# Performance work log

Measured on AMD Instinct MI355X. Metric: run time of the kernel, lower is better.

Reference implementation:

```python
import jax, jax.numpy as jnp
import numpy as np

S, D, A, H, C = 2048, 256, 64, 8, 64  # seq_len, node_dim, num_aux, num_heads, num_channels
QUAT = 4
N_TYPES = 3  # nodes, aux, rot


def _linear_params(key, out_dim, in_dim, use_bias=True):
    kw, kb = jax.random.split(key)
    lim = 1.0 / np.sqrt(in_dim)
    W = jax.random.uniform(kw, (out_dim, in_dim), minval=-lim, maxval=lim, dtype=jnp.float32)
    if not use_bias:
        return W, None
    b = jax.random.uniform(kb, (out_dim,), minval=-lim, maxval=lim, dtype=jnp.float32)
    return W, b


def setup_inputs() -> dict:
    key = jax.random.key(0)
    ks = jax.random.split(key, 8)
    nodes = jax.random.normal(ks[0], (S, D), dtype=jnp.float32)
    aux = jax.random.normal(ks[1], (S, A), dtype=jnp.float32)
    rot = jax.random.normal(ks[2], (S, QUAT), dtype=jnp.float32)
    W_nodes, b_nodes = _linear_params(ks[3], H * C * 2, D)
    W_aux, b_aux = _linear_params(ks[4], H * C * 2, A)
    W_rot, _ = _linear_params(ks[5], H * C * 2, QUAT, use_bias=False)
    W_val, b_val = _linear_params(ks[6], D * H * N_TYPES, D)
    return {
        "nodes": nodes, "aux": aux, "rot": rot,
        "W_nodes": W_nodes, "b_nodes": b_nodes,
        "W_aux": W_aux, "b_aux": b_aux,
        "W_rot": W_rot,
        "W_val": W_val, "b_val": b_val,
    }


def reference(nodes, aux, rot, W_nodes, b_nodes, W_aux, b_aux, W_rot, W_val, b_val):
    seq_len = nodes.shape[0]
    # values: (S, 3H, D)
    val = (nodes @ W_val.T + b_val).reshape(seq_len, N_TYPES * H, -1)
    # per-source k/q: each (S, H, C)
    nodes_k, nodes_q = jnp.split((nodes @ W_nodes.T + b_nodes).reshape(seq_len, H, -1), 2, -1)
    aux_k, aux_q = jnp.split((aux @ W_aux.T + b_aux).reshape(seq_len, H, -1), 2, -1)
    rot_k, rot_q = jnp.split((rot @ W_rot.T).reshape(seq_len, H, -1), 2, -1)
    # concat along head axis -> (S, 3H, C)
    k = jnp.concatenate([nodes_k, aux_k, rot_k], axis=-2)
    q = jnp.concatenate([nodes_q, aux_q, rot_q], axis=-2)
    # (S, S, 3H) score tensor, scaled by 1/sqrt(num_heads) as in the original
    logits = jnp.einsum('ihc,jhc->ijh', k, q) / jnp.sqrt(jnp.asarray(H, nodes.dtype))
    att = jax.nn.softmax(logits, axis=-2)  # softmax over the j (key) axis
    out = jnp.einsum('ijh,jhd->id', att, val)  # (S, D)
    return out
```

## Files before the change

### kernel.cpp

```cpp
#include <hip/hip_runtime.h>

#define S_LEN 2048
#define NHEAD 24
#define CDIM 64
#define DDIM 256

typedef _Float16 f16x8 __attribute__((ext_vector_type(8)));
typedef float f32x4 __attribute__((ext_vector_type(4)));

__device__ __forceinline__ ushort f2h(float f) {
    _Float16 h = (_Float16)f;
    return __builtin_bit_cast(ushort, h);
}
__device__ __forceinline__ uint pkh(float a, float b) {
    auto v = __builtin_amdgcn_cvt_pkrtz(a, b);
    return __builtin_bit_cast(uint, v);
}
__device__ __forceinline__ uint pk2(float a, float b) {
    return (uint)f2h(a) | ((uint)f2h(b) << 16);
}

__device__ __forceinline__ int4 cvt8(const float* __restrict__ p) {
    float4 a = *(const float4*)p;
    float4 b = *(const float4*)(p + 4);
    f16x8 h;
    h[0] = (_Float16)a.x; h[1] = (_Float16)a.y;
    h[2] = (_Float16)a.z; h[3] = (_Float16)a.w;
    h[4] = (_Float16)b.x; h[5] = (_Float16)b.y;
    h[6] = (_Float16)b.z; h[7] = (_Float16)b.w;
    return __builtin_bit_cast(int4, h);
}

__global__ __launch_bounds__(256) void prep_kernel(
    const float* __restrict__ nodes, const float* __restrict__ W_val,
    float* __restrict__ out, ushort* __restrict__ nodes16, ushort* __restrict__ Wval16)
{
    int idx = blockIdx.x * 256 + threadIdx.x;
    if (idx < 131072) {
        ((float4*)out)[idx] = float4{0.f, 0.f, 0.f, 0.f};
    } else if (idx < 196608) {
        int i = idx - 131072;
        *(int4*)&nodes16[i * 8] = cvt8(&nodes[i * 8]);
    } else {
        int i = idx - 196608;
        *(int4*)&Wval16[i * 8] = cvt8(&W_val[i * 8]);
    }
}

__global__ __launch_bounds__(256) void proj_kernel(
    const float* __restrict__ nodes, const float* __restrict__ W_nodes,
    const float* __restrict__ b_nodes,
    const float* __restrict__ aux, const float* __restrict__ W_aux,
    const float* __restrict__ b_aux,
    const float* __restrict__ rot, const float* __restrict__ W_rot,
    const ushort* __restrict__ nodes16, const ushort* __restrict__ Wval16,
    const float* __restrict__ b_val,
    ushort* __restrict__ Kbuf, ushort* __restrict__ Qbuf, ushort* __restrict__ Vt)
{
    __shared__ ushort Asub[128 * 72];
    __shared__ ushort Wsub[128 * 72];
    const int blk = blockIdx.x;
    const int tid = threadIdx.x;
    const int wave = tid >> 6, lane = tid & 63;
    const int g = lane >> 4, c = lane & 15;

    if (blk < 768) {
        const int wm = wave & 1, wn = wave >> 1;
        const int m0 = (blk / 48) * 128, n0 = (blk % 48) * 128;
        const int K = 256;

        f32x4 acc[16];
#pragma unroll
        for (int t = 0; t < 16; t++) acc[t] = f32x4{0, 0, 0, 0};

        for (int k0 = 0; k0 < K; k0 += 64) {
            __syncthreads();
#pragma unroll
            for (int q = 0; q < 4; q++) {
                int i = tid + 256 * q;
                int row = i >> 3, kc = (i & 7) * 8;
                *(int4*)&Asub[row * 72 + kc] = *(const int4*)&nodes16[(m0 + row) * K + k0 + kc];
                *(int4*)&Wsub[row * 72 + kc] = *(const int4*)&Wval16[(n0 + row) * K + k0 + kc];
            }
            __syncthreads();

            f16x8 af0[4], af1[4];
#pragma unroll
            for (int mt = 0; mt < 4; mt++) {
                const ushort* Ar = &Asub[(wm * 64 + mt * 16 + c) * 72 + g * 8];
                af0[mt] = *(const f16x8*)Ar;
                af1[mt] = *(const f16x8*)(Ar + 32);
            }
#pragma unroll
            for (int nt = 0; nt < 4; nt++) {
                const ushort* Wr = &Wsub[(wn * 64 + nt * 16 + c) * 72 + g * 8];
                f16x8 bf0 = *(const f16x8*)Wr;
                f16x8 bf1 = *(const f16x8*)(Wr + 32);
#pragma unroll
                for (int mt = 0; mt < 4; mt++) {
                    acc[mt * 4 + nt] = __builtin_amdgcn_mfma_f32_16x16x32_f16(af0[mt], bf0, acc[mt * 4 + nt], 0, 0, 0);
                    acc[mt * 4 + nt] = __builtin_amdgcn_mfma_f32_16x16x32_f16(af1[mt], bf1, acc[mt * 4 + nt], 0, 0, 0);
                }
            }
        }

#pragma unroll
        for (int nt = 0; nt < 4; nt++) {
            int n = n0 + wn * 64 + nt * 16 + c;
            float bv = b_val[n];
            int h = n >> 8, d = n & 255;
#pragma unroll
            for (int mt = 0; mt < 4; mt++) {
                int m = m0 + wm * 64 + mt * 16 + g * 4;
                f32x4 v = acc[mt * 4 + nt];
                uint2 pw;
                pw.x = pk2(v[0] + bv, v[1] + bv);
                pw.y = pk2(v[2] + bv, v[3] + bv);
                *(uint2*)&Vt[(h * DDIM + d) * S_LEN + m] = pw;
            }
        }
    } else if (blk < 1792) {
        const int sub = blk - 768;
        const float *A, *W, *b;
        int K, hbase;
        if (sub < 512) { A = nodes; W = W_nodes; b = b_nodes; K = 256; hbase = 0; }
        else           { A = aux;   W = W_aux;   b = b_aux;   K = 64;  hbase = 8; }
        const int t5 = sub & 511;
        const int m0 = (t5 >> 4) * 64, n0 = (t5 & 15) * 64;
        const int srow = tid >> 2;
        const int skk = (tid & 3) * 8;

        f32x4 acc[4] = {f32x4{0,0,0,0}, f32x4{0,0,0,0}, f32x4{0,0,0,0}, f32x4{0,0,0,0}};

        for (int k0 = 0; k0 < K; k0 += 32) {
            __syncthreads();
            *(int4*)&Asub[srow * 40 + skk] = cvt8(&A[(m0 + srow) * K + k0 + skk]);
            *(int4*)&Wsub[srow * 40 + skk] = cvt8(&W[(n0 + srow) * K + k0 + skk]);
            __syncthreads();
            f16x8 af = *(const f16x8*)&Asub[(wave * 16 + c) * 40 + g * 8];
#pragma unroll
            for (int t = 0; t < 4; t++) {
                f16x8 bf = *(const f16x8*)&Wsub[(t * 16 + c) * 40 + g * 8];
                acc[t] = __builtin_amdgcn_mfma_f32_16x16x32_f16(af, bf, acc[t], 0, 0, 0);
            }
        }

#pragma unroll
        for (int t = 0; t < 4; t++) {
            int n = n0 + t * 16 + c;
            float bv = b[n];
#pragma unroll
            for (int r = 0; r < 4; r++) {
                int m = m0 + wave * 16 + g * 4 + r;
                ushort u = f2h(acc[t][r] + bv);
                int h = hbase + (n >> 7);
                int cc = n & 127;
                if (cc < 64) Kbuf[(h * S_LEN + m) * CDIM + cc] = u;
                else         Qbuf[(h * S_LEN + m) * CDIM + cc - 64] = u;
            }
        }
    } else {
        int u = (blk - 1792) * 256 + tid;
        int i = u >> 7;
        int n8 = (u & 127) * 8;
        float4 r = *(const float4*)&rot[i * 4];
        ushort pv[8];
#pragma unroll
        for (int q = 0; q < 8; q++) {
            float4 w = *(const float4*)&W_rot[(n8 + q) * 4];
            pv[q] = f2h(r.x * w.x + r.y * w.y + r.z * w.z + r.w * w.w);
        }
        int h = 16 + (n8 >> 7), cc = n8 & 127;
        int4 pkt = *(int4*)pv;
        if (cc < 64) *(int4*)&Kbuf[(h * S_LEN + i) * CDIM + cc] = pkt;
        else         *(int4*)&Qbuf[(h * S_LEN + i) * CDIM + cc - 64] = pkt;
    }
}

__global__ __launch_bounds__(256) void flash_kernel(
    const ushort* __restrict__ Kbuf, const ushort* __restrict__ Qbuf,
    const ushort* __restrict__ Vt, float* __restrict__ out)
{
    __shared__ ushort Qlds[2][64 * 72];
    __shared__ ushort Plds[2][64 * 72];
    __shared__ float  Alds[2][64];

    const int tid = threadIdx.x;
    const int wave = tid >> 6, lane = tid & 63;
    const int g = lane >> 4, c = lane & 15;
    const int h = blockIdx.y;
    const int i0 = blockIdx.x * 64;
    const float SC = 0.51006973f;

    const ushort* Krow = &Kbuf[(h * S_LEN + i0 + wave * 16 + c) * CDIM + g * 8];
    f16x8 ka0 = *(const f16x8*)Krow;
    f16x8 ka1 = *(const f16x8*)(Krow + 32);

    const ushort* Vbase = &Vt[(h * DDIM + wave * 64 + c) * S_LEN + g * 8];

    const int qi0 = tid, qi1 = tid + 256;
    const int qr0 = qi0 >> 3, qc0 = (qi0 & 7) * 8;
    const int qr1 = qi1 >> 3, qc1 = (qi1 & 7) * 8;

    *(int4*)&Qlds[0][qr0 * 72 + qc0] =
        *(const int4*)&Qbuf[(h * S_LEN + qr0) * CDIM + qc0];
    *(int4*)&Qlds[0][qr1 * 72 + qc1] =
        *(const int4*)&Qbuf[(h * S_LEN + qr1) * CDIM + qc1];
    __syncthreads();

    f32x4 acc[16];
#pragma unroll
    for (int t = 0; t < 16; t++) acc[t] = f32x4{0, 0, 0, 0};
    float mrow = -1e30f, lrow = 0.f;

    for (int j0 = 0; j0 < S_LEN; j0 += 64) {
        const int cur = (j0 >> 6) & 1, nxt = cur ^ 1;

        const int jn = j0 + 64;
        int4 qn0 = *(const int4*)&Qbuf[(h * S_LEN + jn + qr0) * CDIM + qc0];
        int4 qn1 = *(const int4*)&Qbuf[(h * S_LEN + jn + qr1) * CDIM + qc1];

        f16x8 vf0[4], vf1[4];
#pragma unroll
        for (int t = 0; t < 4; t++) {
            const ushort* Vr = Vbase + (t * 16) * S_LEN + j0;
            vf0[t] = *(const f16x8*)Vr;
            vf1[t] = *(const f16x8*)(Vr + 32);
        }

        f32x4 Sf[4];
#pragma unroll
        for (int jc = 0; jc < 4; jc++) {
            const ushort* Qr = &Qlds[cur][(jc * 16 + c) * 72 + g * 8];
            f16x8 qb0 = *(const f16x8*)Qr;
            f16x8 qb1 = *(const f16x8*)(Qr + 32);
            f32x4 s = {0, 0, 0, 0};
            s = __builtin_amdgcn_mfma_f32_16x16x32_f16(qb0, ka0, s, 0, 0, 0);
            s = __builtin_amdgcn_mfma_f32_16x16x32_f16(qb1, ka1, s, 0, 0, 0);
            Sf[jc] = s * SC;
        }

        float nm = -1e30f;
#pragma unroll
        for (int jc = 0; jc < 4; jc++)
            nm = fmaxf(nm, fmaxf(fmaxf(Sf[jc][0], Sf[jc][1]),
                                 fmaxf(Sf[jc][2], Sf[jc][3])));
        nm = fmaxf(nm, __shfl_xor(nm, 16));
        nm = fmaxf(nm, __shfl_xor(nm, 32));
        nm = fmaxf(nm, mrow);
        float alpha = exp2f(mrow - nm);

        float rs = 0.f;
#pragma unroll
        for (int jc = 0; jc < 4; jc++) {
            float p0 = exp2f(Sf[jc][0] - nm);
            float p1 = exp2f(Sf[jc][1] - nm);
            float p2 = exp2f(Sf[jc][2] - nm);
            float p3 = exp2f(Sf[jc][3] - nm);
            rs += (p0 + p1) + (p2 + p3);
            uint2 w;
            w.x = pkh(p0, p1);
            w.y = pkh(p2, p3);
            *(uint2*)&Plds[cur][(wave * 16 + c) * 72 + jc * 16 + g * 4] = w;
        }
        rs += __shfl_xor(rs, 16);
        rs += __shfl_xor(rs, 32);
        lrow = lrow * alpha + rs;
        mrow = nm;
        if (g == 0) Alds[cur][wave * 16 + c] = alpha;

        *(int4*)&Qlds[nxt][qr0 * 72 + qc0] = qn0;
        *(int4*)&Qlds[nxt][qr1 * 72 + qc1] = qn1;

        __syncthreads();

#pragma unroll
        for (int b = 0; b < 4; b++) {
            f32x4 ab = *(const f32x4*)&Alds[cur][b * 16 + g * 4];
#pragma unroll
            for (int t = 0; t < 4; t++) acc[b * 4 + t] *= ab;
        }

#pragma unroll
        for (int b = 0; b < 4; b++) {
            const ushort* Pr = &Plds[cur][(b * 16 + c) * 72 + g * 8];
            f16x8 pa0 = *(const f16x8*)Pr;
            f16x8 pa1 = *(const f16x8*)(Pr + 32);
#pragma unroll
            for (int t = 0; t < 4; t++) {
                acc[b * 4 + t] = __builtin_amdgcn_mfma_f32_16x16x32_f16(pa0, vf0[t], acc[b * 4 + t], 0, 0, 0);
                acc[b * 4 + t] = __builtin_amdgcn_mfma_f32_16x16x32_f16(pa1, vf1[t], acc[b * 4 + t], 0, 0, 0);
            }
        }
    }

    __syncthreads();
    if (g == 0) Alds[0][wave * 16 + c] = 1.0f / lrow;
    __syncthreads();
#pragma unroll
    for (int b = 0; b < 4; b++) {
        f32x4 lb = *(const f32x4*)&Alds[0][b * 16 + g * 4];
#pragma unroll
        for (int t = 0; t < 4; t++)
#pragma unroll
            for (int r = 0; r < 4; r++) {
                int i = i0 + b * 16 + g * 4 + r;
                int d = wave * 64 + t * 16 + c;
                atomicAdd(&out[i * DDIM + d], acc[b * 4 + t][r] * lb[r]);
            }
    }
}

extern "C" void kernel_launch(void* const* d_in, const int* in_sizes, int n_in,
                              void* d_out, int out_size, void* d_ws, size_t ws_size,
                              hipStream_t stream) {
    const float *nodes = 0, *aux = 0, *rot = 0, *W_nodes = 0, *b_nodes = 0,
                *W_aux = 0, *b_aux = 0, *W_rot = 0, *W_val = 0, *b_val = 0;
    int i1024[2] = {-1, -1};
    int n1024 = 0;
    for (int i = 0; i < n_in; ++i) {
        const float* p = (const float*)d_in[i];
        switch (in_sizes[i]) {
            case 524288:  nodes   = p; break;
            case 131072:  aux     = p; break;
            case 8192:    rot     = p; break;
            case 262144:  W_nodes = p; break;
            case 65536:   W_aux   = p; break;
            case 4096:    W_rot   = p; break;
            case 1572864: W_val   = p; break;
            case 6144:    b_val   = p; break;
            case 1024:    if (n1024 < 2) i1024[n1024] = i; n1024++; break;
            default: break;
        }
    }
    if (n1024 == 2) {
        b_nodes = (const float*)d_in[i1024[0]];
        b_aux   = (const float*)d_in[i1024[1]];
    }
    if (!nodes || !aux || !rot || !W_nodes || !b_nodes || !W_aux || !b_aux ||
        !W_rot || !W_val || !b_val) {
        nodes   = (const float*)d_in[0];
        aux     = (const float*)d_in[1];
        rot     = (const float*)d_in[2];
        W_nodes = (const float*)d_in[3];
        b_nodes = (const float*)d_in[4];
        W_aux   = (const float*)d_in[5];
        b_aux   = (const float*)d_in[6];
        W_rot   = (const float*)d_in[7];
        W_val   = (const float*)d_in[8];
        b_val   = (const float*)d_in[9];
    }
    float* out = (float*)d_out;

    float*  Opad = (float*)d_ws;
    ushort* Kbuf = (ushort*)(Opad + S_LEN * DDIM);
    ushort* Qbuf = Kbuf + NHEAD * S_LEN * CDIM;
    ushort* Vt   = Qbuf + NHEAD * S_LEN * CDIM;
    ushort* nodes16 = Vt + NHEAD * DDIM * S_LEN;
    ushort* Wval16  = nodes16 + 524288;

    dim3 blk(256);
    prep_kernel<<<dim3(1536), blk, 0, stream>>>(nodes, W_val, out, nodes16, Wval16);
    proj_kernel<<<dim3(2816), blk, 0, stream>>>(
        nodes, W_nodes, b_nodes, aux, W_aux, b_aux, rot, W_rot,
        nodes16, Wval16, b_val, Kbuf, Qbuf, Vt);
    flash_kernel<<<dim3(32, NHEAD), blk, 0, stream>>>(Kbuf, Qbuf, Vt, out);
}
```

Measured before the change: 253.5 us.

## Route K/Q projections through tiled fp16 GEMM, fold softmax scale into K

```diff
diff --git a/kernel.cpp b/kernel.cpp
--- a/kernel.cpp
+++ b/kernel.cpp
@@ -8,6 +8,8 @@
 typedef _Float16 f16x8 __attribute__((ext_vector_type(8)));
 typedef float f32x4 __attribute__((ext_vector_type(4)));
 
+#define SCALE 0.51006973f
+
 __device__ __forceinline__ ushort f2h(float f) {
     _Float16 h = (_Float16)f;
     return __builtin_bit_cast(ushort, h);
@@ -16,10 +18,6 @@
     auto v = __builtin_amdgcn_cvt_pkrtz(a, b);
     return __builtin_bit_cast(uint, v);
 }
-__device__ __forceinline__ uint pk2(float a, float b) {
-    return (uint)f2h(a) | ((uint)f2h(b) << 16);
-}
-
 __device__ __forceinline__ int4 cvt8(const float* __restrict__ p) {
     float4 a = *(const float4*)p;
     float4 b = *(const float4*)(p + 4);
@@ -33,7 +31,11 @@
 
 __global__ __launch_bounds__(256) void prep_kernel(
     const float* __restrict__ nodes, const float* __restrict__ W_val,
-    float* __restrict__ out, ushort* __restrict__ nodes16, ushort* __restrict__ Wval16)
+    const float* __restrict__ W_nodes, const float* __restrict__ aux,
+    const float* __restrict__ W_aux,
+    float* __restrict__ out, ushort* __restrict__ nodes16,
+    ushort* __restrict__ Wval16, ushort* __restrict__ Wnodes16,
+    ushort* __restrict__ aux16, ushort* __restrict__ Waux16)
 {
     int idx = blockIdx.x * 256 + threadIdx.x;
     if (idx < 131072) {
@@ -41,33 +43,54 @@
     } else if (idx < 196608) {
         int i = idx - 131072;
         *(int4*)&nodes16[i * 8] = cvt8(&nodes[i * 8]);
-    } else {
+    } else if (idx < 393216) {
         int i = idx - 196608;
         *(int4*)&Wval16[i * 8] = cvt8(&W_val[i * 8]);
+    } else if (idx < 425984) {
+        int i = idx - 393216;
+        *(int4*)&Wnodes16[i * 8] = cvt8(&W_nodes[i * 8]);
+    } else if (idx < 442368) {
+        int i = idx - 425984;
+        *(int4*)&aux16[i * 8] = cvt8(&aux[i * 8]);
+    } else if (idx < 450560) {
+        int i = idx - 442368;
+        *(int4*)&Waux16[i * 8] = cvt8(&W_aux[i * 8]);
     }
 }
 
 __global__ __launch_bounds__(256) void proj_kernel(
-    const float* __restrict__ nodes, const float* __restrict__ W_nodes,
-    const float* __restrict__ b_nodes,
-    const float* __restrict__ aux, const float* __restrict__ W_aux,
-    const float* __restrict__ b_aux,
     const float* __restrict__ rot, const float* __restrict__ W_rot,
     const ushort* __restrict__ nodes16, const ushort* __restrict__ Wval16,
-    const float* __restrict__ b_val,
+    const ushort* __restrict__ Wnodes16, const ushort* __restrict__ aux16,
+    const ushort* __restrict__ Waux16,
+    const float* __restrict__ b_val, const float* __restrict__ b_nodes,
+    const float* __restrict__ b_aux,
     ushort* __restrict__ Kbuf, ushort* __restrict__ Qbuf, ushort* __restrict__ Vt)
 {
-    __shared__ ushort Asub[128 * 72];
-    __shared__ ushort Wsub[128 * 72];
+    __shared__ ushort Asub[128 * 66];
+    __shared__ ushort Wsub[128 * 66];
     const int blk = blockIdx.x;
     const int tid = threadIdx.x;
     const int wave = tid >> 6, lane = tid & 63;
     const int g = lane >> 4, c = lane & 15;
 
-    if (blk < 768) {
+    if (blk < 1024) {
+        const ushort *A16, *W16;
+        const float* bias;
+        int K, m0, n0, mode, hbase = 0;
+        if (blk < 768) {
+            A16 = nodes16; W16 = Wval16; bias = b_val; K = 256; mode = 0;
+            m0 = (blk / 48) * 128; n0 = (blk % 48) * 128;
+        } else if (blk < 896) {
+            int sub = blk - 768;
+            A16 = nodes16; W16 = Wnodes16; bias = b_nodes; K = 256; mode = 1; hbase = 0;
+            m0 = (sub >> 3) * 128; n0 = (sub & 7) * 128;
+        } else {
+            int sub = blk - 896;
+            A16 = aux16; W16 = Waux16; bias = b_aux; K = 64; mode = 1; hbase = 8;
+            m0 = (sub >> 3) * 128; n0 = (sub & 7) * 128;
+        }
         const int wm = wave & 1, wn = wave >> 1;
-        const int m0 = (blk / 48) * 128, n0 = (blk % 48) * 128;
-        const int K = 256;
 
         f32x4 acc[16];
 #pragma unroll
@@ -79,21 +102,21 @@
             for (int q = 0; q < 4; q++) {
                 int i = tid + 256 * q;
                 int row = i >> 3, kc = (i & 7) * 8;
-                *(int4*)&Asub[row * 72 + kc] = *(const int4*)&nodes16[(m0 + row) * K + k0 + kc];
-                *(int4*)&Wsub[row * 72 + kc] = *(const int4*)&Wval16[(n0 + row) * K + k0 + kc];
+                *(int4*)&Asub[row * 66 + kc] = *(const int4*)&A16[(m0 + row) * K + k0 + kc];
+                *(int4*)&Wsub[row * 66 + kc] = *(const int4*)&W16[(n0 + row) * K + k0 + kc];
             }
             __syncthreads();
 
             f16x8 af0[4], af1[4];
 #pragma unroll
             for (int mt = 0; mt < 4; mt++) {
-                const ushort* Ar = &Asub[(wm * 64 + mt * 16 + c) * 72 + g * 8];
+                const ushort* Ar = &Asub[(wm * 64 + mt * 16 + c) * 66 + g * 8];
                 af0[mt] = *(const f16x8*)Ar;
                 af1[mt] = *(const f16x8*)(Ar + 32);
             }
 #pragma unroll
             for (int nt = 0; nt < 4; nt++) {
-                const ushort* Wr = &Wsub[(wn * 64 + nt * 16 + c) * 72 + g * 8];
+                const ushort* Wr = &Wsub[(wn * 64 + nt * 16 + c) * 66 + g * 8];
                 f16x8 bf0 = *(const f16x8*)Wr;
                 f16x8 bf1 = *(const f16x8*)(Wr + 32);
 #pragma unroll
@@ -104,76 +127,59 @@
             }
         }
 
-#pragma unroll
-        for (int nt = 0; nt < 4; nt++) {
-            int n = n0 + wn * 64 + nt * 16 + c;
-            float bv = b_val[n];
-            int h = n >> 8, d = n & 255;
-#pragma unroll
-            for (int mt = 0; mt < 4; mt++) {
-                int m = m0 + wm * 64 + mt * 16 + g * 4;
-                f32x4 v = acc[mt * 4 + nt];
-                uint2 pw;
-                pw.x = pk2(v[0] + bv, v[1] + bv);
-                pw.y = pk2(v[2] + bv, v[3] + bv);
-                *(uint2*)&Vt[(h * DDIM + d) * S_LEN + m] = pw;
-            }
-        }
-    } else if (blk < 1792) {
-        const int sub = blk - 768;
-        const float *A, *W, *b;
-        int K, hbase;
-        if (sub < 512) { A = nodes; W = W_nodes; b = b_nodes; K = 256; hbase = 0; }
-        else           { A = aux;   W = W_aux;   b = b_aux;   K = 64;  hbase = 8; }
-        const int t5 = sub & 511;
-        const int m0 = (t5 >> 4) * 64, n0 = (t5 & 15) * 64;
-        const int srow = tid >> 2;
-        const int skk = (tid & 3) * 8;
-
-        f32x4 acc[4] = {f32x4{0,0,0,0}, f32x4{0,0,0,0}, f32x4{0,0,0,0}, f32x4{0,0,0,0}};
-
-        for (int k0 = 0; k0 < K; k0 += 32) {
-            __syncthreads();
-            *(int4*)&Asub[srow * 40 + skk] = cvt8(&A[(m0 + srow) * K + k0 + skk]);
-            *(int4*)&Wsub[srow * 40 + skk] = cvt8(&W[(n0 + srow) * K + k0 + skk]);
-            __syncthreads();
-            f16x8 af = *(const f16x8*)&Asub[(wave * 16 + c) * 40 + g * 8];
-#pragma unroll
-            for (int t = 0; t < 4; t++) {
-                f16x8 bf = *(const f16x8*)&Wsub[(t * 16 + c) * 40 + g * 8];
-                acc[t] = __builtin_amdgcn_mfma_f32_16x16x32_f16(af, bf, acc[t], 0, 0, 0);
-            }
-        }
-
-#pragma unroll
-        for (int t = 0; t < 4; t++) {
-            int n = n0 + t * 16 + c;
-            float bv = b[n];
-#pragma unroll
-            for (int r = 0; r < 4; r++) {
-                int m = m0 + wave * 16 + g * 4 + r;
-                ushort u = f2h(acc[t][r] + bv);
+        if (mode == 0) {
+#pragma unroll
+            for (int nt = 0; nt < 4; nt++) {
+                int n = n0 + wn * 64 + nt * 16 + c;
+                float bv = bias[n];
+                int h = n >> 8, d = n & 255;
+#pragma unroll
+                for (int mt = 0; mt < 4; mt++) {
+                    int m = m0 + wm * 64 + mt * 16 + g * 4;
+                    f32x4 v = acc[mt * 4 + nt];
+                    uint2 pw;
+                    pw.x = pkh(v[0] + bv, v[1] + bv);
+                    pw.y = pkh(v[2] + bv, v[3] + bv);
+                    *(uint2*)&Vt[(h * DDIM + d) * S_LEN + m] = pw;
+                }
+            }
+        } else {
+#pragma unroll
+            for (int nt = 0; nt < 4; nt++) {
+                int n = n0 + wn * 64 + nt * 16 + c;
+                float bv = bias[n];
                 int h = hbase + (n >> 7);
                 int cc = n & 127;
-                if (cc < 64) Kbuf[(h * S_LEN + m) * CDIM + cc] = u;
-                else         Qbuf[(h * S_LEN + m) * CDIM + cc - 64] = u;
+#pragma unroll
+                for (int mt = 0; mt < 4; mt++) {
+                    int m = m0 + wm * 64 + mt * 16 + g * 4;
+                    f32x4 v = acc[mt * 4 + nt];
+#pragma unroll
+                    for (int r = 0; r < 4; r++) {
+                        float x = v[r] + bv;
+                        if (cc < 64) Kbuf[(h * S_LEN + m + r) * CDIM + cc] = f2h(x * SCALE);
+                        else         Qbuf[(h * S_LEN + m + r) * CDIM + cc - 64] = f2h(x);
+                    }
+                }
             }
         }
     } else {
-        int u = (blk - 1792) * 256 + tid;
+        int u = (blk - 1024) * 256 + tid;
         int i = u >> 7;
         int n8 = (u & 127) * 8;
         float4 r = *(const float4*)&rot[i * 4];
+        bool isk = (n8 & 64) == 0;
+        float sc = isk ? SCALE : 1.0f;
         ushort pv[8];
 #pragma unroll
         for (int q = 0; q < 8; q++) {
             float4 w = *(const float4*)&W_rot[(n8 + q) * 4];
-            pv[q] = f2h(r.x * w.x + r.y * w.y + r.z * w.z + r.w * w.w);
+            pv[q] = f2h((r.x * w.x + r.y * w.y + r.z * w.z + r.w * w.w) * sc);
         }
         int h = 16 + (n8 >> 7), cc = n8 & 127;
         int4 pkt = *(int4*)pv;
-        if (cc < 64) *(int4*)&Kbuf[(h * S_LEN + i) * CDIM + cc] = pkt;
-        else         *(int4*)&Qbuf[(h * S_LEN + i) * CDIM + cc - 64] = pkt;
+        if (isk) *(int4*)&Kbuf[(h * S_LEN + i) * CDIM + cc] = pkt;
+        else     *(int4*)&Qbuf[(h * S_LEN + i) * CDIM + cc - 64] = pkt;
     }
 }
 
@@ -181,8 +187,8 @@
     const ushort* __restrict__ Kbuf, const ushort* __restrict__ Qbuf,
     const ushort* __restrict__ Vt, float* __restrict__ out)
 {
-    __shared__ ushort Qlds[2][64 * 72];
-    __shared__ ushort Plds[2][64 * 72];
+    __shared__ ushort Qlds[2][64 * 66];
+    __shared__ ushort Plds[2][64 * 66];
     __shared__ float  Alds[2][64];
 
     const int tid = threadIdx.x;
@@ -190,7 +196,6 @@
     const int g = lane >> 4, c = lane & 15;
     const int h = blockIdx.y;
     const int i0 = blockIdx.x * 64;
-    const float SC = 0.51006973f;
 
     const ushort* Krow = &Kbuf[(h * S_LEN + i0 + wave * 16 + c) * CDIM + g * 8];
     f16x8 ka0 = *(const f16x8*)Krow;
@@ -202,9 +207,9 @@
     const int qr0 = qi0 >> 3, qc0 = (qi0 & 7) * 8;
     const int qr1 = qi1 >> 3, qc1 = (qi1 & 7) * 8;
 
-    *(int4*)&Qlds[0][qr0 * 72 + qc0] =
+    *(int4*)&Qlds[0][qr0 * 66 + qc0] =
         *(const int4*)&Qbuf[(h * S_LEN + qr0) * CDIM + qc0];
-    *(int4*)&Qlds[0][qr1 * 72 + qc1] =
+    *(int4*)&Qlds[0][qr1 * 66 + qc1] =
         *(const int4*)&Qbuf[(h * S_LEN + qr1) * CDIM + qc1];
     __syncthreads();
 
@@ -231,13 +236,13 @@
         f32x4 Sf[4];
 #pragma unroll
         for (int jc = 0; jc < 4; jc++) {
-            const ushort* Qr = &Qlds[cur][(jc * 16 + c) * 72 + g * 8];
+            const ushort* Qr = &Qlds[cur][(jc * 16 + c) * 66 + g * 8];
             f16x8 qb0 = *(const f16x8*)Qr;
             f16x8 qb1 = *(const f16x8*)(Qr + 32);
             f32x4 s = {0, 0, 0, 0};
             s = __builtin_amdgcn_mfma_f32_16x16x32_f16(qb0, ka0, s, 0, 0, 0);
             s = __builtin_amdgcn_mfma_f32_16x16x32_f16(qb1, ka1, s, 0, 0, 0);
-            Sf[jc] = s * SC;
+            Sf[jc] = s;
         }
 
         float nm = -1e30f;
@@ -261,7 +266,7 @@
             uint2 w;
             w.x = pkh(p0, p1);
             w.y = pkh(p2, p3);
-            *(uint2*)&Plds[cur][(wave * 16 + c) * 72 + jc * 16 + g * 4] = w;
+            *(uint2*)&Plds[cur][(wave * 16 + c) * 66 + jc * 16 + g * 4] = w;
         }
         rs += __shfl_xor(rs, 16);
         rs += __shfl_xor(rs, 32);
@@ -269,8 +274,8 @@
         mrow = nm;
         if (g == 0) Alds[cur][wave * 16 + c] = alpha;
 
-        *(int4*)&Qlds[nxt][qr0 * 72 + qc0] = qn0;
-        *(int4*)&Qlds[nxt][qr1 * 72 + qc1] = qn1;
+        *(int4*)&Qlds[nxt][qr0 * 66 + qc0] = qn0;
+        *(int4*)&Qlds[nxt][qr1 * 66 + qc1] = qn1;
 
         __syncthreads();
 
@@ -283,7 +288,7 @@
 
 #pragma unroll
         for (int b = 0; b < 4; b++) {
-            const ushort* Pr = &Plds[cur][(b * 16 + c) * 72 + g * 8];
+            const ushort* Pr = &Plds[cur][(b * 16 + c) * 66 + g * 8];
             f16x8 pa0 = *(const f16x8*)Pr;
             f16x8 pa1 = *(const f16x8*)(Pr + 32);
 #pragma unroll
@@ -356,13 +361,18 @@
     ushort* Kbuf = (ushort*)(Opad + S_LEN * DDIM);
     ushort* Qbuf = Kbuf + NHEAD * S_LEN * CDIM;
     ushort* Vt   = Qbuf + NHEAD * S_LEN * CDIM;
-    ushort* nodes16 = Vt + NHEAD * DDIM * S_LEN;
-    ushort* Wval16  = nodes16 + 524288;
+    ushort* nodes16  = Vt + NHEAD * DDIM * S_LEN;
+    ushort* Wval16   = nodes16 + 524288;
+    ushort* Wnodes16 = Wval16 + 1572864;
+    ushort* aux16    = Wnodes16 + 262144;
+    ushort* Waux16   = aux16 + 131072;
 
     dim3 blk(256);
-    prep_kernel<<<dim3(1536), blk, 0, stream>>>(nodes, W_val, out, nodes16, Wval16);
-    proj_kernel<<<dim3(2816), blk, 0, stream>>>(
-        nodes, W_nodes, b_nodes, aux, W_aux, b_aux, rot, W_rot,
-        nodes16, Wval16, b_val, Kbuf, Qbuf, Vt);
+    prep_kernel<<<dim3(1760), blk, 0, stream>>>(
+        nodes, W_val, W_nodes, aux, W_aux,
+        out, nodes16, Wval16, Wnodes16, aux16, Waux16);
+    proj_kernel<<<dim3(2048), blk, 0, stream>>>(
+        rot, W_rot, nodes16, Wval16, Wnodes16, aux16, Waux16,
+        b_val, b_nodes, b_aux, Kbuf, Qbuf, Vt);
     flash_kernel<<<dim3(32, NHEAD), blk, 0, stream>>>(Kbuf, Qbuf, Vt, out);
 }
```

Measured after the change: 348.6 us. +37.5%, slower.
